# Optimization experiments

Measured on AMD Instinct MI355X. Metric: run time of the kernel, lower is better.

## Reference

```python
import jax, jax.numpy as jnp
import numpy as np

SCALE = 0.125  # quantization scale applied inline in the custom matmul
PAD = 4
STRIDE = 1


def setup_inputs() -> dict:
    key = jax.random.key(0)
    k1, k2, k3 = jax.random.split(key, 3)
    x = jax.random.normal(k1, (8, 64, 16384), dtype=jnp.float32)        # (N, C, L)
    weight = jax.random.normal(k2, (64, 64, 9), dtype=jnp.float32) * 0.05  # (O, I, K)
    bias = jax.random.normal(k3, (64,), dtype=jnp.float32)               # (O,)
    return {"x": x, "weight": weight, "bias": bias}


def reference(x, weight, bias):
    # Mathematically identical to: im2col unfold -> (N, out_l, C*K) @ (C*K, O),
    # then out * scale + bias. Expressed as a fused conv to avoid the huge
    # intermediate while computing the same result.
    out = jax.lax.conv_general_dilated(
        x, weight,
        window_strides=(STRIDE,),
        padding=[(PAD, PAD)],
        dimension_numbers=("NCH", "OIH", "NCH"),
    )  # (N, O, out_l)
    return out * SCALE + bias[None, :, None]
```

## Files before the change

kernel.cpp:

```cpp
#include <hip/hip_runtime.h>
#include <hip/hip_bf16.h>

#define C_IN    64
#define L_IN    16384
#define O_OUT   64
#define KTAP    9
#define LTILE   128
#define ROWS    144
#define RSTRIDE 72

typedef short          bf16x8 __attribute__((ext_vector_type(8)));
typedef unsigned short u16x8  __attribute__((ext_vector_type(8)));
typedef unsigned int   u32x4  __attribute__((ext_vector_type(4)));
typedef float          f32x4  __attribute__((ext_vector_type(4)));
typedef float          f32x8v __attribute__((ext_vector_type(8)));

static __device__ __forceinline__ unsigned short f2bf(float f) {
  __hip_bfloat16 h = __float2bfloat16(f);
  return __builtin_bit_cast(unsigned short, h);
}

static __device__ __forceinline__ unsigned int pk2(float lo, float hi) {
  return (unsigned int)f2bf(lo) | ((unsigned int)f2bf(hi) << 16);
}

__global__ void w_rearrange(const float* __restrict__ w,
                            unsigned short* __restrict__ w2) {
    int i = blockIdx.x * 256 + threadIdx.x;
    if (i >= KTAP * O_OUT * C_IN) return;
    int t  = i >> 12;
    int oc = i & 4095;
    w2[i] = f2bf(w[oc * KTAP + t] * 0.125f);
}

__global__ __launch_bounds__(256) void qconv_kernel(
    const float* __restrict__ x,
    const unsigned short* __restrict__ w2,
    const float* __restrict__ bias,
    float* __restrict__ out) {

  __shared__ __align__(16) unsigned short xs[ROWS][RSTRIDE];

  const int tid = threadIdx.x;
  const int n   = blockIdx.x >> 7;
  const int l0  = (blockIdx.x & 127) << 7;
  const float* xn = x + (size_t)n * C_IN * L_IN;

  for (int idx = tid; idx < ROWS; idx += 256) {
    const int cb = idx & 7;
    const int lb = idx >> 3;
    const int c0 = cb << 3;
    const int gl0 = l0 - 8 + (lb << 3);
    if (gl0 >= 0 && gl0 + 8 <= L_IN) {
      f32x8v v[8];
#pragma unroll
      for (int i = 0; i < 8; ++i)
        v[i] = *reinterpret_cast<const f32x8v*>(xn + (size_t)(c0 + i) * L_IN + gl0);
#pragma unroll
      for (int j = 0; j < 8; ++j) {
        u32x4 wv;
#pragma unroll
        for (int p = 0; p < 4; ++p)
          wv[p] = pk2(v[2 * p][j], v[2 * p + 1][j]);
        *reinterpret_cast<u32x4*>(&xs[(lb << 3) + j][c0]) = wv;
      }
    } else {
      unsigned short vb[8][8];
      for (int i = 0; i < 8; ++i)
        for (int j = 0; j < 8; ++j) {
          int gl = gl0 + j;
          vb[i][j] = (gl >= 0 && gl < L_IN)
                         ? f2bf(xn[(size_t)(c0 + i) * L_IN + gl])
                         : (unsigned short)0;
        }
      for (int j = 0; j < 8; ++j) {
        u16x8 wv;
        for (int i = 0; i < 8; ++i) wv[i] = vb[i][j];
        *reinterpret_cast<u16x8*>(&xs[(lb << 3) + j][c0]) = wv;
      }
    }
  }
  __syncthreads();

  const int wave = tid >> 6;
  const int lane = tid & 63;
  const int wr   = wave >> 1;
  const int wc   = wave & 1;
  const int col  = lane & 15;
  const int quad = lane >> 4;

  f32x4 acc[2][4];
#pragma unroll
  for (int m = 0; m < 2; ++m)
#pragma unroll
    for (int lt = 0; lt < 4; ++lt) acc[m][lt] = (f32x4){0.f, 0.f, 0.f, 0.f};

  const int rbase = (wc << 6) + col + 4;

  for (int t = 0; t < KTAP; ++t) {
    bf16x8 a[2][2];
#pragma unroll
    for (int m = 0; m < 2; ++m)
#pragma unroll
      for (int k = 0; k < 2; ++k)
        a[m][k] = *reinterpret_cast<const bf16x8*>(
            w2 + (t << 12) + (((wr << 5) + (m << 4) + col) << 6) + (k << 5) + (quad << 3));

#pragma unroll
    for (int k = 0; k < 2; ++k) {
#pragma unroll
      for (int lt = 0; lt < 4; ++lt) {
        const int r = rbase + t + (lt << 4);
        const bf16x8 b = *reinterpret_cast<const bf16x8*>(&xs[r][(k << 5) + (quad << 3)]);
        acc[0][lt] = __builtin_amdgcn_mfma_f32_16x16x32_bf16(a[0][k], b, acc[0][lt], 0, 0, 0);
        acc[1][lt] = __builtin_amdgcn_mfma_f32_16x16x32_bf16(a[1][k], b, acc[1][lt], 0, 0, 0);
      }
    }
  }

#pragma unroll
  for (int m = 0; m < 2; ++m) {
    const int obase = (wr << 5) + (m << 4) + (quad << 2);
    float bv[4];
#pragma unroll
    for (int reg = 0; reg < 4; ++reg) bv[reg] = bias[obase + reg];
#pragma unroll
    for (int lt = 0; lt < 4; ++lt) {
      const int l = l0 + (wc << 6) + (lt << 4) + col;
#pragma unroll
      for (int reg = 0; reg < 4; ++reg) {
        const int o = obase + reg;
        out[((size_t)(n * O_OUT + o) << 14) + l] = acc[m][lt][reg] + bv[reg];
      }
    }
  }
}

extern "C" void kernel_launch(void* const* d_in, const int* in_sizes, int n_in,
                              void* d_out, int out_size, void* d_ws, size_t ws_size,
                              hipStream_t stream) {
  const float*    x    = (const float*)d_in[0];
  const float*    w    = (const float*)d_in[1];
  const float*    bias = (const float*)d_in[2];
  float*          out  = (float*)d_out;
  unsigned short* w2   = (unsigned short*)d_ws;

  w_rearrange<<<(KTAP * O_OUT * C_IN + 255) / 256, 256, 0, stream>>>(w, w2);

  qconv_kernel<<<8 * (L_IN / LTILE), 256, 0, stream>>>(x, w2, bias, out);
}
```

Baseline: 112.4 us.

## Process two L-halves per block, overlapping second-half load with first-half MFMA

Each block now covers 256 output positions in two halves of 128. The first half's input tile is staged into shared memory up front. The second half's extra rows are loaded into registers during the first half's MFMA loop and written to shared memory once the first half no longer reads those rows. Weight fragments are double-buffered (prefetching tap t+2) and bias is hoisted. This trades half as many blocks and more registers for hiding global-load latency behind compute.

```diff
diff --git a/kernel.cpp b/kernel.cpp
--- a/kernel.cpp
+++ b/kernel.cpp
@@ -5,12 +5,12 @@
 #define L_IN    16384
 #define O_OUT   64
 #define KTAP    9
-#define LTILE   128
-#define ROWS    144
+#define LTILE   256
+#define ROWS    272
+#define ROWS_A  144
 #define RSTRIDE 72
 
 typedef short          bf16x8 __attribute__((ext_vector_type(8)));
-typedef unsigned short u16x8  __attribute__((ext_vector_type(8)));
 typedef unsigned int   u32x4  __attribute__((ext_vector_type(4)));
 typedef float          f32x4  __attribute__((ext_vector_type(4)));
 typedef float          f32x8v __attribute__((ext_vector_type(8)));
@@ -19,7 +19,6 @@
   __hip_bfloat16 h = __float2bfloat16(f);
   return __builtin_bit_cast(unsigned short, h);
 }
-
 static __device__ __forceinline__ unsigned int pk2(float lo, float hi) {
   return (unsigned int)f2bf(lo) | ((unsigned int)f2bf(hi) << 16);
 }
@@ -33,6 +32,35 @@
     w2[i] = f2bf(w[oc * KTAP + t] * 0.125f);
 }
 
+static __device__ __forceinline__ void load_unit(const float* __restrict__ xn,
+                                                 int l0, int lb, int cb,
+                                                 f32x8v v[8]) {
+  const int c0  = cb << 3;
+  const int gl0 = l0 - 8 + (lb << 3);
+  if (gl0 >= 0 && gl0 + 8 <= L_IN) {
+#pragma unroll
+    for (int i = 0; i < 8; ++i)
+      v[i] = *reinterpret_cast<const f32x8v*>(xn + (size_t)(c0 + i) * L_IN + gl0);
+  } else {
+    for (int i = 0; i < 8; ++i)
+      for (int j = 0; j < 8; ++j) {
+        int gl = gl0 + j;
+        v[i][j] = (gl >= 0 && gl < L_IN) ? xn[(size_t)(c0 + i) * L_IN + gl] : 0.f;
+      }
+  }
+}
+static __device__ __forceinline__ void write_unit(unsigned short xs[ROWS][RSTRIDE],
+                                                  int lb, int cb, const f32x8v v[8]) {
+  const int c0 = cb << 3;
+#pragma unroll
+  for (int j = 0; j < 8; ++j) {
+    u32x4 wv;
+#pragma unroll
+    for (int p = 0; p < 4; ++p) wv[p] = pk2(v[2 * p][j], v[2 * p + 1][j]);
+    *reinterpret_cast<u32x4*>(&xs[(lb << 3) + j][c0]) = wv;
+  }
+}
+
 __global__ __launch_bounds__(256) void qconv_kernel(
     const float* __restrict__ x,
     const unsigned short* __restrict__ w2,
@@ -42,45 +70,9 @@
   __shared__ __align__(16) unsigned short xs[ROWS][RSTRIDE];
 
   const int tid = threadIdx.x;
-  const int n   = blockIdx.x >> 7;
-  const int l0  = (blockIdx.x & 127) << 7;
+  const int n   = blockIdx.x >> 6;
+  const int l0  = (blockIdx.x & 63) << 8;
   const float* xn = x + (size_t)n * C_IN * L_IN;
-
-  for (int idx = tid; idx < ROWS; idx += 256) {
-    const int cb = idx & 7;
-    const int lb = idx >> 3;
-    const int c0 = cb << 3;
-    const int gl0 = l0 - 8 + (lb << 3);
-    if (gl0 >= 0 && gl0 + 8 <= L_IN) {
-      f32x8v v[8];
-#pragma unroll
-      for (int i = 0; i < 8; ++i)
-        v[i] = *reinterpret_cast<const f32x8v*>(xn + (size_t)(c0 + i) * L_IN + gl0);
-#pragma unroll
-      for (int j = 0; j < 8; ++j) {
-        u32x4 wv;
-#pragma unroll
-        for (int p = 0; p < 4; ++p)
-          wv[p] = pk2(v[2 * p][j], v[2 * p + 1][j]);
-        *reinterpret_cast<u32x4*>(&xs[(lb << 3) + j][c0]) = wv;
-      }
-    } else {
-      unsigned short vb[8][8];
-      for (int i = 0; i < 8; ++i)
-        for (int j = 0; j < 8; ++j) {
-          int gl = gl0 + j;
-          vb[i][j] = (gl >= 0 && gl < L_IN)
-                         ? f2bf(xn[(size_t)(c0 + i) * L_IN + gl])
-                         : (unsigned short)0;
-        }
-      for (int j = 0; j < 8; ++j) {
-        u16x8 wv;
-        for (int i = 0; i < 8; ++i) wv[i] = vb[i][j];
-        *reinterpret_cast<u16x8*>(&xs[(lb << 3) + j][c0]) = wv;
-      }
-    }
-  }
-  __syncthreads();
 
   const int wave = tid >> 6;
   const int lane = tid & 63;
@@ -89,51 +81,101 @@
   const int col  = lane & 15;
   const int quad = lane >> 4;
 
+  if (tid < ROWS_A) {
+    f32x8v va[8];
+    load_unit(xn, l0, tid >> 3, tid & 7, va);
+    write_unit(xs, tid >> 3, tid & 7, va);
+  }
+  __syncthreads();
+
+  float bv[2][4];
+#pragma unroll
+  for (int m = 0; m < 2; ++m)
+#pragma unroll
+    for (int reg = 0; reg < 4; ++reg)
+      bv[m][reg] = bias[(wr << 5) + (m << 4) + (quad << 2) + reg];
+
+  const unsigned short* wbase = w2 + ((((wr << 5) + col) << 6) + (quad << 3));
+  auto lda = [&](bf16x8 a[2][2], int t) {
+#pragma unroll
+    for (int m = 0; m < 2; ++m)
+#pragma unroll
+      for (int k = 0; k < 2; ++k)
+        a[m][k] = *reinterpret_cast<const bf16x8*>(wbase + (t << 12) + (m << 10) + (k << 5));
+  };
+
+  auto kstep = [&](int h, int t, const bf16x8 a[2][2], f32x4 acc[2][4]) {
+    const int rb = (h << 7) + (wc << 6) + col + 4 + t;
+#pragma unroll
+    for (int k = 0; k < 2; ++k)
+#pragma unroll
+      for (int lt = 0; lt < 4; ++lt) {
+        const bf16x8 b =
+            *reinterpret_cast<const bf16x8*>(&xs[rb + (lt << 4)][(k << 5) + (quad << 3)]);
+        acc[0][lt] = __builtin_amdgcn_mfma_f32_16x16x32_bf16(a[0][k], b, acc[0][lt], 0, 0, 0);
+        acc[1][lt] = __builtin_amdgcn_mfma_f32_16x16x32_bf16(a[1][k], b, acc[1][lt], 0, 0, 0);
+      }
+  };
+
+  auto epi = [&](int h, const f32x4 acc[2][4]) {
+#pragma unroll
+    for (int m = 0; m < 2; ++m) {
+      const int obase = (wr << 5) + (m << 4) + (quad << 2);
+#pragma unroll
+      for (int lt = 0; lt < 4; ++lt) {
+        const int l = l0 + (h << 7) + (wc << 6) + (lt << 4) + col;
+#pragma unroll
+        for (int reg = 0; reg < 4; ++reg)
+          out[((size_t)(n * O_OUT + obase + reg) << 14) + l] = acc[m][lt][reg] + bv[m][reg];
+      }
+    }
+  };
+
+  bf16x8 ac[2][2], an[2][2];
+  lda(ac, 0);
+  lda(an, 1);
+
+  const bool actB = tid < 128;
+  f32x8v vbuf[8];
+  if (actB) load_unit(xn, l0, 18 + (tid >> 3), tid & 7, vbuf);
+
   f32x4 acc[2][4];
 #pragma unroll
   for (int m = 0; m < 2; ++m)
 #pragma unroll
     for (int lt = 0; lt < 4; ++lt) acc[m][lt] = (f32x4){0.f, 0.f, 0.f, 0.f};
 
-  const int rbase = (wc << 6) + col + 4;
-
+#pragma unroll
   for (int t = 0; t < KTAP; ++t) {
-    bf16x8 a[2][2];
+    kstep(0, t, ac, acc);
 #pragma unroll
     for (int m = 0; m < 2; ++m)
 #pragma unroll
-      for (int k = 0; k < 2; ++k)
-        a[m][k] = *reinterpret_cast<const bf16x8*>(
-            w2 + (t << 12) + (((wr << 5) + (m << 4) + col) << 6) + (k << 5) + (quad << 3));
+      for (int k = 0; k < 2; ++k) ac[m][k] = an[m][k];
+    if (t + 2 < KTAP) lda(an, t + 2);
+    if (t == 1 && actB)
+      write_unit(xs, 18 + (tid >> 3), tid & 7, vbuf);
+  }
+  epi(0, acc);
+  __syncthreads();
+
+  lda(ac, 0);
+  lda(an, 1);
+#pragma unroll
+  for (int m = 0; m < 2; ++m)
+#pragma unroll
+    for (int lt = 0; lt < 4; ++lt) acc[m][lt] = (f32x4){0.f, 0.f, 0.f, 0.f};
 
 #pragma unroll
-    for (int k = 0; k < 2; ++k) {
+  for (int t = 0; t < KTAP; ++t) {
+    kstep(1, t, ac, acc);
 #pragma unroll
-      for (int lt = 0; lt < 4; ++lt) {
-        const int r = rbase + t + (lt << 4);
-        const bf16x8 b = *reinterpret_cast<const bf16x8*>(&xs[r][(k << 5) + (quad << 3)]);
-        acc[0][lt] = __builtin_amdgcn_mfma_f32_16x16x32_bf16(a[0][k], b, acc[0][lt], 0, 0, 0);
-        acc[1][lt] = __builtin_amdgcn_mfma_f32_16x16x32_bf16(a[1][k], b, acc[1][lt], 0, 0, 0);
-      }
-    }
+    for (int m = 0; m < 2; ++m)
+#pragma unroll
+      for (int k = 0; k < 2; ++k) ac[m][k] = an[m][k];
+    if (t + 2 < KTAP) lda(an, t + 2);
   }
-
-#pragma unroll
-  for (int m = 0; m < 2; ++m) {
-    const int obase = (wr << 5) + (m << 4) + (quad << 2);
-    float bv[4];
-#pragma unroll
-    for (int reg = 0; reg < 4; ++reg) bv[reg] = bias[obase + reg];
-#pragma unroll
-    for (int lt = 0; lt < 4; ++lt) {
-      const int l = l0 + (wc << 6) + (lt << 4) + col;
-#pragma unroll
-      for (int reg = 0; reg < 4; ++reg) {
-        const int o = obase + reg;
-        out[((size_t)(n * O_OUT + o) << 14) + l] = acc[m][lt][reg] + bv[reg];
-      }
-    }
-  }
+  epi(1, acc);
 }
 
 extern "C" void kernel_launch(void* const* d_in, const int* in_sizes, int n_in,
@@ -146,6 +188,5 @@
   unsigned short* w2   = (unsigned short*)d_ws;
 
   w_rearrange<<<(KTAP * O_OUT * C_IN + 255) / 256, 256, 0, stream>>>(w, w2);
-
   qconv_kernel<<<8 * (L_IN / LTILE), 256, 0, stream>>>(x, w2, bias, out);
 }
```

Result: faster. 103.3 us (-8.1%).
